# Kernel optimization log

Hardware: AMD Instinct MI355X
Metric: run time of the kernel (lower is better)

The kernel has to match this reference:

```python
import jax, jax.numpy as jnp
import numpy as np

BS = 4096
IN_DIM = 2048
N = 16384          # out_dim / number of labels
K = 32
D = 2 * K + 1      # 65 frequency components (1 DC + K complex pairs)
SLACK = 64
TOTAL_D = D + SLACK
SQRT2 = np.sqrt(2.0).astype(np.float32)


def setup_inputs() -> dict:
    key = jax.random.key(0)
    k1, k2, k3, k4 = jax.random.split(key, 4)
    x = jax.random.normal(k1, (BS, IN_DIM), dtype=jnp.float32)
    # proj: Linear(in_dim, total_D) with bias
    W_proj = jax.random.normal(k2, (TOTAL_D, IN_DIM), dtype=jnp.float32) / np.sqrt(IN_DIM).astype(np.float32)
    b_proj = jnp.zeros((TOTAL_D,), dtype=jnp.float32)
    # use_init: bias[0] = logit(k/N) * sqrt(N)
    mle = K / N
    b0 = np.float32(np.log(mle / (1.0 - mle)) * np.sqrt(N))
    b_proj = b_proj.at[0].set(b0)
    # Ws: Linear(slack_dims, N, bias=False) -> weight (N, slack_dims)
    Ws = jax.random.normal(k3, (N, SLACK), dtype=jnp.float32) / np.sqrt(SLACK).astype(np.float32)
    return {"x": x, "W_proj": W_proj, "b_proj": b_proj, "Ws": Ws}


def reference(x, W_proj, b_proj, Ws):
    bs = x.shape[0]
    h = x @ W_proj.T + b_proj                      # (bs, TOTAL_D)
    # scale cols 1:D by sqrt(2), leave DC and slack cols untouched
    scale = jnp.concatenate([
        jnp.ones((1,), jnp.float32),
        jnp.full((D - 1,), SQRT2, jnp.float32),
        jnp.ones((SLACK,), jnp.float32),
    ])
    h = h * scale
    dc = h[:, 0]                                   # (bs,)
    pairs = h[:, 1:D].reshape(bs, K, 2)            # (bs, K, 2) [real, imag]
    cx = pairs[:, :, 0] - 1j * pairs[:, :, 1]      # conj of complex(real, imag)
    cx = jnp.concatenate([dc[:, None].astype(cx.dtype), cx], axis=1)  # (bs, K+1)
    # zero-padded orthonormal inverse DFT; only real part kept
    yy_dft = jnp.fft.ifft(cx, n=N, norm='ortho', axis=-1).real        # (bs, N)
    yy_slack = h[:, D:] @ Ws.T                     # (bs, N)
    return yy_dft + yy_slack
```

## Files before the change

### kernel.cpp

```cpp
#include <hip/hip_runtime.h>

#define BS 4096
#define IN_DIM 2048
#define NFFT 16384
#define TOTAL_D 129
#define SLACK 64
#define KF 128
#define NPROJ 160
#define SPLITK 8

#define INV_N_SQRT 0.0078125f
#define SC_PAIR 0.011048543456039804f
#define TWO_PI_OVER_N 3.8349519697141029e-4f

typedef __attribute__((ext_vector_type(8))) short bf16x8;
typedef __attribute__((ext_vector_type(4))) float f32x4;

__device__ __forceinline__ ushort f2bf(float f) {
    union { float f; unsigned u; } v; v.f = f;
    unsigned r = v.u + 0x7fffu + ((v.u >> 16) & 1u);
    return (ushort)(r >> 16);
}

__global__ __launch_bounds__(256) void k_basis(const float* __restrict__ Ws,
                                               ushort* __restrict__ Bb) {
    int idx = blockIdx.x * 256 + threadIdx.x;
    int t = idx >> 4, g = idx & 15;
    ushort r[8];
    if (g < 8) {
#pragma unroll
        for (int p = 0; p < 4; ++p) {
            int f = 4 * g + p + 1;
            int phase = (f * t) & (NFFT - 1);
            float ang = (float)phase * TWO_PI_OVER_N;
            float sv, cv;
            __sincosf(ang, &sv, &cv);
            r[2 * p] = f2bf(cv);
            r[2 * p + 1] = f2bf(sv);
        }
    } else {
        const float* w = &Ws[(size_t)t * SLACK + (g - 8) * 8];
        float4 w0 = *(const float4*)w;
        float4 w1 = *(const float4*)(w + 4);
        r[0] = f2bf(w0.x); r[1] = f2bf(w0.y); r[2] = f2bf(w0.z); r[3] = f2bf(w0.w);
        r[4] = f2bf(w1.x); r[5] = f2bf(w1.y); r[6] = f2bf(w1.z); r[7] = f2bf(w1.w);
    }
    ushort4 lo = {r[0], r[1], r[2], r[3]};
    ushort4 hi = {r[4], r[5], r[6], r[7]};
    ushort* dst = &Bb[(size_t)t * KF + g * 8];
    *(ushort4*)dst = lo;
    *(ushort4*)(dst + 4) = hi;
}

__global__ __launch_bounds__(256, 2) void k_proj(const float* __restrict__ x,
                                                 const float* __restrict__ W,
                                                 float* __restrict__ hp) {
    __shared__ ushort As[128 * 40];
    __shared__ ushort Bs[160 * 40];
    const int tid = threadIdx.x;
    const int lane = tid & 63, wave = tid >> 6;
    const int quad = lane >> 4, m = lane & 15;
    const int wm = wave & 1, wn = wave >> 1;
    const int r0 = blockIdx.x * 128;
    const int kbase = blockIdx.y * (IN_DIM / SPLITK);

    f32x4 acc[4][5];
#pragma unroll
    for (int i = 0; i < 4; ++i)
#pragma unroll
        for (int j = 0; j < 5; ++j) acc[i][j] = 0.f;

    for (int ch = 0; ch < IN_DIM / SPLITK / 32; ++ch) {
        const int kb = kbase + ch * 32;
#pragma unroll
        for (int it = 0; it < 4; ++it) {
            int v = tid + it * 256;
            int row = v >> 3, c = v & 7;
            float4 xv = *(const float4*)&x[(size_t)(r0 + row) * IN_DIM + kb + c * 4];
            ushort4 o = {f2bf(xv.x), f2bf(xv.y), f2bf(xv.z), f2bf(xv.w)};
            *(ushort4*)&As[row * 40 + c * 4] = o;
        }
#pragma unroll
        for (int it = 0; it < 5; ++it) {
            int v = tid + it * 256;
            int row = v >> 3, c = v & 7;
            int rw = row < TOTAL_D ? row : TOTAL_D - 1;
            float4 wv = *(const float4*)&W[(size_t)rw * IN_DIM + kb + c * 4];
            ushort4 o = {f2bf(wv.x), f2bf(wv.y), f2bf(wv.z), f2bf(wv.w)};
            *(ushort4*)&Bs[row * 40 + c * 4] = o;
        }
        __syncthreads();
        bf16x8 af[4], bfr[5];
#pragma unroll
        for (int i = 0; i < 4; ++i)
            af[i] = *(const bf16x8*)&As[(wm * 64 + i * 16 + m) * 40 + quad * 8];
#pragma unroll
        for (int j = 0; j < 5; ++j)
            bfr[j] = *(const bf16x8*)&Bs[(wn * 80 + j * 16 + m) * 40 + quad * 8];
#pragma unroll
        for (int i = 0; i < 4; ++i)
#pragma unroll
            for (int j = 0; j < 5; ++j)
                acc[i][j] = __builtin_amdgcn_mfma_f32_16x16x32_bf16(af[i], bfr[j], acc[i][j], 0, 0, 0);
        __syncthreads();
    }
#pragma unroll
    for (int i = 0; i < 4; ++i)
#pragma unroll
        for (int reg = 0; reg < 4; ++reg) {
            int row = r0 + wm * 64 + i * 16 + quad * 4 + reg;
            float* orow = &hp[((size_t)blockIdx.y * BS + row) * NPROJ + wn * 80 + m];
#pragma unroll
            for (int j = 0; j < 5; ++j) orow[j * 16] = acc[i][j][reg];
        }
}

__global__ __launch_bounds__(256) void k_finalize(const float* __restrict__ hp,
                                                  const float* __restrict__ bvec,
                                                  float* __restrict__ dc0,
                                                  ushort* __restrict__ hs) {
    int b = blockIdx.x * 256 + threadIdx.x;
    int g = blockIdx.y;
    int c0 = g * 8;
    float v[8];
#pragma unroll
    for (int e = 0; e < 8; ++e) v[e] = 0.f;
#pragma unroll
    for (int s = 0; s < SPLITK; ++s) {
        const float* p = &hp[((size_t)s * BS + b) * NPROJ + c0];
        float4 p0 = *(const float4*)p;
        float4 p1 = *(const float4*)(p + 4);
        v[0] += p0.x; v[1] += p0.y; v[2] += p0.z; v[3] += p0.w;
        v[4] += p1.x; v[5] += p1.y; v[6] += p1.z; v[7] += p1.w;
    }
#pragma unroll
    for (int e = 0; e < 8; ++e) {
        int c = c0 + e;
        if (c >= TOTAL_D) break;
        float val = v[e] + bvec[c];
        if (c == 0) {
            dc0[b] = val * INV_N_SQRT;
        } else {
            int k = c - 1;
            float sc = (k < 64) ? SC_PAIR : 1.f;
            hs[(size_t)b * KF + k] = f2bf(val * sc);
        }
    }
}

__global__ __launch_bounds__(256, 2) void k_main(const ushort* __restrict__ hs,
                                                 const float* __restrict__ dc0,
                                                 const ushort* __restrict__ Bb,
                                                 float* __restrict__ out) {
    __shared__ ushort As[128 * 128];
    __shared__ ushort Bs[128 * 128];
    const int tid = threadIdx.x;
    const int lane = tid & 63, wave = tid >> 6;
    const int quad = lane >> 4, m = lane & 15;
    const int wm = wave & 1, wn = wave >> 1;
    const int t0 = blockIdx.x * 128;
    const int b0 = blockIdx.y * 128;

#pragma unroll
    for (int it = 0; it < 8; ++it) {
        int v = tid + it * 256;
        int row = v >> 4, g = v & 15;
        uint4 d = *(const uint4*)&Bb[((size_t)(t0 + row) << 7) + g * 8];
        *(uint4*)&As[(row << 7) + ((g ^ (row & 7)) * 8)] = d;
    }
#pragma unroll
    for (int it = 0; it < 8; ++it) {
        int v = tid + it * 256;
        int row = v >> 4, g = v & 15;
        uint4 d = *(const uint4*)&hs[((size_t)(b0 + row) << 7) + g * 8];
        *(uint4*)&Bs[(row << 7) + ((g ^ (row & 7)) * 8)] = d;
    }

    f32x4 acc[4][4];
#pragma unroll
    for (int j = 0; j < 4; ++j) {
        float d = dc0[b0 + wn * 64 + j * 16 + m];
#pragma unroll
        for (int i = 0; i < 4; ++i) acc[i][j] = d;
    }
    __syncthreads();

#pragma unroll
    for (int ks = 0; ks < 4; ++ks) {
        bf16x8 af[4], bfr[4];
#pragma unroll
        for (int i = 0; i < 4; ++i) {
            int row = wm * 64 + i * 16 + m;
            af[i] = *(const bf16x8*)&As[(row << 7) + (((ks * 4 + quad) ^ (row & 7)) * 8)];
        }
#pragma unroll
        for (int j = 0; j < 4; ++j) {
            int row = wn * 64 + j * 16 + m;
            bfr[j] = *(const bf16x8*)&Bs[(row << 7) + (((ks * 4 + quad) ^ (row & 7)) * 8)];
        }
#pragma unroll
        for (int i = 0; i < 4; ++i)
#pragma unroll
            for (int j = 0; j < 4; ++j)
                acc[i][j] = __builtin_amdgcn_mfma_f32_16x16x32_bf16(af[i], bfr[j], acc[i][j], 0, 0, 0);
    }

#pragma unroll
    for (int j = 0; j < 4; ++j) {
        size_t rowb = (size_t)(b0 + wn * 64 + j * 16 + m);
        float* orow = out + rowb * NFFT + t0 + wm * 64 + quad * 4;
#pragma unroll
        for (int i = 0; i < 4; ++i)
            *(f32x4*)&orow[i * 16] = acc[i][j];
    }
}

extern "C" void kernel_launch(void* const* d_in, const int* in_sizes, int n_in,
                              void* d_out, int out_size, void* d_ws, size_t ws_size,
                              hipStream_t stream) {
    const float* x   = (const float*)d_in[0];
    const float* W   = (const float*)d_in[1];
    const float* b   = (const float*)d_in[2];
    const float* Wsl = (const float*)d_in[3];
    float* out = (float*)d_out;

    char* ws = (char*)d_ws;
    float*  h_part = (float*)ws;
    ushort* Bb     = (ushort*)(ws + 20971520);
    ushort* hs     = (ushort*)(ws + 25165824);
    float*  dc0    = (float*)(ws + 26214400);

    k_basis<<<NFFT * 16 / 256, 256, 0, stream>>>(Wsl, Bb);
    k_proj<<<dim3(BS / 128, SPLITK), 256, 0, stream>>>(x, W, h_part);
    k_finalize<<<dim3(BS / 256, 17), 256, 0, stream>>>(h_part, b, dc0, hs);
    k_main<<<dim3(NFFT / 128, BS / 128), 256, 0, stream>>>(hs, dc0, Bb, out);
}
```

Measured before the change: 335.6 us.

## Load GEMM fragments directly from global, remap blocks for XCD locality, nontemporal stores

The output GEMM kernel no longer stages A/B tiles in shared memory. Each wave loads its MFMA fragments straight from global/L2, which removes LDS traffic and the barrier and allows 4 blocks per CU. The grid is flattened and remapped so blocks on the same XCD share basis tiles, and output writes use nontemporal stores to avoid polluting cache. The trade-off is that fragment loads are now redundant across waves and go through global memory with less coalescing.

```diff
diff --git a/kernel.cpp b/kernel.cpp
--- a/kernel.cpp
+++ b/kernel.cpp
@@ -148,33 +148,23 @@
     }
 }
 
-__global__ __launch_bounds__(256, 2) void k_main(const ushort* __restrict__ hs,
+__global__ __launch_bounds__(256, 4) void k_main(const ushort* __restrict__ hs,
                                                  const float* __restrict__ dc0,
                                                  const ushort* __restrict__ Bb,
                                                  float* __restrict__ out) {
-    __shared__ ushort As[128 * 128];
-    __shared__ ushort Bs[128 * 128];
     const int tid = threadIdx.x;
     const int lane = tid & 63, wave = tid >> 6;
     const int quad = lane >> 4, m = lane & 15;
     const int wm = wave & 1, wn = wave >> 1;
-    const int t0 = blockIdx.x * 128;
-    const int b0 = blockIdx.y * 128;
-
-#pragma unroll
-    for (int it = 0; it < 8; ++it) {
-        int v = tid + it * 256;
-        int row = v >> 4, g = v & 15;
-        uint4 d = *(const uint4*)&Bb[((size_t)(t0 + row) << 7) + g * 8];
-        *(uint4*)&As[(row << 7) + ((g ^ (row & 7)) * 8)] = d;
-    }
-#pragma unroll
-    for (int it = 0; it < 8; ++it) {
-        int v = tid + it * 256;
-        int row = v >> 4, g = v & 15;
-        uint4 d = *(const uint4*)&hs[((size_t)(b0 + row) << 7) + g * 8];
-        *(uint4*)&Bs[(row << 7) + ((g ^ (row & 7)) * 8)] = d;
-    }
+
+    int orig = blockIdx.x;
+    int wgid = ((orig & 7) << 9) + (orig >> 3);
+    int tx = wgid >> 5, by = wgid & 31;
+    const int t0 = tx * 128;
+    const int b0 = by * 128;
+
+    const ushort* pA = Bb + (((size_t)(t0 + wm * 64 + m)) << 7) + quad * 8;
+    const ushort* pB = hs + (((size_t)(b0 + wn * 64 + m)) << 7) + quad * 8;
 
     f32x4 acc[4][4];
 #pragma unroll
@@ -183,21 +173,16 @@
 #pragma unroll
         for (int i = 0; i < 4; ++i) acc[i][j] = d;
     }
-    __syncthreads();
 
 #pragma unroll
     for (int ks = 0; ks < 4; ++ks) {
         bf16x8 af[4], bfr[4];
 #pragma unroll
-        for (int i = 0; i < 4; ++i) {
-            int row = wm * 64 + i * 16 + m;
-            af[i] = *(const bf16x8*)&As[(row << 7) + (((ks * 4 + quad) ^ (row & 7)) * 8)];
-        }
-#pragma unroll
-        for (int j = 0; j < 4; ++j) {
-            int row = wn * 64 + j * 16 + m;
-            bfr[j] = *(const bf16x8*)&Bs[(row << 7) + (((ks * 4 + quad) ^ (row & 7)) * 8)];
-        }
+        for (int i = 0; i < 4; ++i)
+            af[i] = *(const bf16x8*)(pA + (size_t)i * 16 * KF + ks * 32);
+#pragma unroll
+        for (int j = 0; j < 4; ++j)
+            bfr[j] = *(const bf16x8*)(pB + (size_t)j * 16 * KF + ks * 32);
 #pragma unroll
         for (int i = 0; i < 4; ++i)
 #pragma unroll
@@ -211,7 +196,7 @@
         float* orow = out + rowb * NFFT + t0 + wm * 64 + quad * 4;
 #pragma unroll
         for (int i = 0; i < 4; ++i)
-            *(f32x4*)&orow[i * 16] = acc[i][j];
+            __builtin_nontemporal_store(acc[i][j], (f32x4*)&orow[i * 16]);
     }
 }
 
@@ -233,5 +218,5 @@
     k_basis<<<NFFT * 16 / 256, 256, 0, stream>>>(Wsl, Bb);
     k_proj<<<dim3(BS / 128, SPLITK), 256, 0, stream>>>(x, W, h_part);
     k_finalize<<<dim3(BS / 256, 17), 256, 0, stream>>>(h_part, b, dc0, hs);
-    k_main<<<dim3(NFFT / 128, BS / 128), 256, 0, stream>>>(hs, dc0, Bb, out);
-}
+    k_main<<<NFFT / 128 * (BS / 128), 256, 0, stream>>>(hs, dc0, Bb, out);
+}
```

Result: slower. 410.3 us (+22.3%).

## Loop k_main over four t-tiles per block with prefetched basis and remapped grid

Applied to the files above, without the earlier changes.

Each k_main block now covers 128 batch rows by 512 output columns. It keeps the hs tile resident in LDS and loops over four basis tiles, loading the next basis tile into registers while the current one is computed and stored. A 1D grid with an XCD-aware block remap groups blocks for L2 locality. This aims to cut redundant hs loads and per-block launch and prologue cost, at the price of extra barriers, higher register pressure and a quarter as many blocks.

```diff
diff --git a/kernel.cpp b/kernel.cpp
--- a/kernel.cpp
+++ b/kernel.cpp
@@ -158,60 +158,93 @@
     const int lane = tid & 63, wave = tid >> 6;
     const int quad = lane >> 4, m = lane & 15;
     const int wm = wave & 1, wn = wave >> 1;
-    const int t0 = blockIdx.x * 128;
-    const int b0 = blockIdx.y * 128;
-
+
+    int orig = blockIdx.x;
+    int wg = ((orig & 7) << 7) + (orig >> 3);
+    const int b0 = (wg & 31) * 128;
+    const int tbase = (wg >> 5) * 512;
+
+    const int srow = tid >> 4;
+    const int sgr = tid & 15;
+
+    uint4 rh[8], rb[8];
 #pragma unroll
     for (int it = 0; it < 8; ++it) {
-        int v = tid + it * 256;
-        int row = v >> 4, g = v & 15;
-        uint4 d = *(const uint4*)&Bb[((size_t)(t0 + row) << 7) + g * 8];
-        *(uint4*)&As[(row << 7) + ((g ^ (row & 7)) * 8)] = d;
+        int row = srow + it * 16;
+        rh[it] = *(const uint4*)&hs[((size_t)(b0 + row) << 7) + sgr * 8];
     }
 #pragma unroll
     for (int it = 0; it < 8; ++it) {
-        int v = tid + it * 256;
-        int row = v >> 4, g = v & 15;
-        uint4 d = *(const uint4*)&hs[((size_t)(b0 + row) << 7) + g * 8];
-        *(uint4*)&Bs[(row << 7) + ((g ^ (row & 7)) * 8)] = d;
-    }
-
-    f32x4 acc[4][4];
-#pragma unroll
-    for (int j = 0; j < 4; ++j) {
-        float d = dc0[b0 + wn * 64 + j * 16 + m];
-#pragma unroll
-        for (int i = 0; i < 4; ++i) acc[i][j] = d;
-    }
+        int row = srow + it * 16;
+        rb[it] = *(const uint4*)&Bb[((size_t)(tbase + row) << 7) + sgr * 8];
+    }
+#pragma unroll
+    for (int it = 0; it < 8; ++it) {
+        int row = srow + it * 16;
+        int gx = (sgr ^ (row & 7)) * 8;
+        *(uint4*)&Bs[(row << 7) + gx] = rh[it];
+        *(uint4*)&As[(row << 7) + gx] = rb[it];
+    }
+    float dc[4];
+#pragma unroll
+    for (int j = 0; j < 4; ++j) dc[j] = dc0[b0 + wn * 64 + j * 16 + m];
     __syncthreads();
 
-#pragma unroll
-    for (int ks = 0; ks < 4; ++ks) {
-        bf16x8 af[4], bfr[4];
-#pragma unroll
-        for (int i = 0; i < 4; ++i) {
-            int row = wm * 64 + i * 16 + m;
-            af[i] = *(const bf16x8*)&As[(row << 7) + (((ks * 4 + quad) ^ (row & 7)) * 8)];
-        }
+#pragma unroll 1
+    for (int i = 0; i < 4; ++i) {
+        const int t0 = tbase + i * 128;
+        if (i < 3) {
+#pragma unroll
+            for (int it = 0; it < 8; ++it) {
+                int row = srow + it * 16;
+                rb[it] = *(const uint4*)&Bb[((size_t)(t0 + 128 + row) << 7) + sgr * 8];
+            }
+        }
+
+        f32x4 acc[4][4];
+#pragma unroll
+        for (int j = 0; j < 4; ++j)
+#pragma unroll
+            for (int ii = 0; ii < 4; ++ii) acc[ii][j] = dc[j];
+
+#pragma unroll
+        for (int ks = 0; ks < 4; ++ks) {
+            bf16x8 af[4], bfr[4];
+#pragma unroll
+            for (int ii = 0; ii < 4; ++ii) {
+                int row = wm * 64 + ii * 16 + m;
+                af[ii] = *(const bf16x8*)&As[(row << 7) + (((ks * 4 + quad) ^ (row & 7)) * 8)];
+            }
+#pragma unroll
+            for (int j = 0; j < 4; ++j) {
+                int row = wn * 64 + j * 16 + m;
+                bfr[j] = *(const bf16x8*)&Bs[(row << 7) + (((ks * 4 + quad) ^ (row & 7)) * 8)];
+            }
+#pragma unroll
+            for (int ii = 0; ii < 4; ++ii)
+#pragma unroll
+                for (int j = 0; j < 4; ++j)
+                    acc[ii][j] = __builtin_amdgcn_mfma_f32_16x16x32_bf16(af[ii], bfr[j], acc[ii][j], 0, 0, 0);
+        }
+
 #pragma unroll
         for (int j = 0; j < 4; ++j) {
-            int row = wn * 64 + j * 16 + m;
-            bfr[j] = *(const bf16x8*)&Bs[(row << 7) + (((ks * 4 + quad) ^ (row & 7)) * 8)];
-        }
-#pragma unroll
-        for (int i = 0; i < 4; ++i)
-#pragma unroll
-            for (int j = 0; j < 4; ++j)
-                acc[i][j] = __builtin_amdgcn_mfma_f32_16x16x32_bf16(af[i], bfr[j], acc[i][j], 0, 0, 0);
-    }
-
-#pragma unroll
-    for (int j = 0; j < 4; ++j) {
-        size_t rowb = (size_t)(b0 + wn * 64 + j * 16 + m);
-        float* orow = out + rowb * NFFT + t0 + wm * 64 + quad * 4;
-#pragma unroll
-        for (int i = 0; i < 4; ++i)
-            *(f32x4*)&orow[i * 16] = acc[i][j];
+            size_t rowb = (size_t)(b0 + wn * 64 + j * 16 + m);
+            float* orow = out + rowb * NFFT + t0 + wm * 64 + quad * 4;
+#pragma unroll
+            for (int ii = 0; ii < 4; ++ii)
+                *(f32x4*)&orow[ii * 16] = acc[ii][j];
+        }
+
+        if (i < 3) {
+            __syncthreads();
+#pragma unroll
+            for (int it = 0; it < 8; ++it) {
+                int row = srow + it * 16;
+                *(uint4*)&As[(row << 7) + ((sgr ^ (row & 7)) * 8)] = rb[it];
+            }
+            __syncthreads();
+        }
     }
 }
 
@@ -233,5 +266,5 @@
     k_basis<<<NFFT * 16 / 256, 256, 0, stream>>>(Wsl, Bb);
     k_proj<<<dim3(BS / 128, SPLITK), 256, 0, stream>>>(x, W, h_part);
     k_finalize<<<dim3(BS / 256, 17), 256, 0, stream>>>(h_part, b, dc0, hs);
-    k_main<<<dim3(NFFT / 128, BS / 128), 256, 0, stream>>>(hs, dc0, Bb, out);
-}
+    k_main<<<BS / 128 * (NFFT / 512), 256, 0, stream>>>(hs, dc0, Bb, out);
+}
```

Measured after the change: 396.1 us. +18.0%, slower.

## Fuse projection and finalize into one kernel, dropping split-K partial buffer

Applied to the files above, without the earlier changes.

Replaces the split-K projection GEMM and separate reduction/finalize kernel with one kernel in which each block computes 32 rows over the full K dimension and applies bias, scaling and bf16 conversion in its epilogue. This removes the 21MB partial-sum write and re-read and one launch. The trade-off is that every block now re-reads and re-converts the full W_proj matrix (160x2048) from global memory, with only 128 blocks and no split-K parallelism, so the W traffic grows and the per-block serial K loop is longer.

```diff
diff --git a/kernel.cpp b/kernel.cpp
--- a/kernel.cpp
+++ b/kernel.cpp
@@ -6,8 +6,6 @@
 #define TOTAL_D 129
 #define SLACK 64
 #define KF 128
-#define NPROJ 160
-#define SPLITK 8
 
 #define INV_N_SQRT 0.0078125f
 #define SC_PAIR 0.011048543456039804f
@@ -52,98 +50,71 @@
     *(ushort4*)(dst + 4) = hi;
 }
 
-__global__ __launch_bounds__(256, 2) void k_proj(const float* __restrict__ x,
+__global__ __launch_bounds__(256) void k_projfin(const float* __restrict__ x,
                                                  const float* __restrict__ W,
-                                                 float* __restrict__ hp) {
-    __shared__ ushort As[128 * 40];
-    __shared__ ushort Bs[160 * 40];
+                                                 const float* __restrict__ bvec,
+                                                 float* __restrict__ dc0,
+                                                 ushort* __restrict__ hs) {
+    __shared__ ushort As[32 * 72];
+    __shared__ ushort Bs[160 * 72];
     const int tid = threadIdx.x;
     const int lane = tid & 63, wave = tid >> 6;
     const int quad = lane >> 4, m = lane & 15;
     const int wm = wave & 1, wn = wave >> 1;
-    const int r0 = blockIdx.x * 128;
-    const int kbase = blockIdx.y * (IN_DIM / SPLITK);
-
-    f32x4 acc[4][5];
-#pragma unroll
-    for (int i = 0; i < 4; ++i)
-#pragma unroll
-        for (int j = 0; j < 5; ++j) acc[i][j] = 0.f;
-
-    for (int ch = 0; ch < IN_DIM / SPLITK / 32; ++ch) {
-        const int kb = kbase + ch * 32;
-#pragma unroll
-        for (int it = 0; it < 4; ++it) {
+    const int r0 = blockIdx.x * 32;
+
+    f32x4 acc[5];
+#pragma unroll
+    for (int j = 0; j < 5; ++j) acc[j] = 0.f;
+
+    for (int kb = 0; kb < IN_DIM; kb += 64) {
+#pragma unroll
+        for (int it = 0; it < 2; ++it) {
             int v = tid + it * 256;
-            int row = v >> 3, c = v & 7;
+            int row = v >> 4, c = v & 15;
             float4 xv = *(const float4*)&x[(size_t)(r0 + row) * IN_DIM + kb + c * 4];
             ushort4 o = {f2bf(xv.x), f2bf(xv.y), f2bf(xv.z), f2bf(xv.w)};
-            *(ushort4*)&As[row * 40 + c * 4] = o;
-        }
-#pragma unroll
-        for (int it = 0; it < 5; ++it) {
+            *(ushort4*)&As[row * 72 + c * 4] = o;
+        }
+#pragma unroll
+        for (int it = 0; it < 10; ++it) {
             int v = tid + it * 256;
-            int row = v >> 3, c = v & 7;
+            int row = v >> 4, c = v & 15;
             int rw = row < TOTAL_D ? row : TOTAL_D - 1;
             float4 wv = *(const float4*)&W[(size_t)rw * IN_DIM + kb + c * 4];
             ushort4 o = {f2bf(wv.x), f2bf(wv.y), f2bf(wv.z), f2bf(wv.w)};
-            *(ushort4*)&Bs[row * 40 + c * 4] = o;
+            *(ushort4*)&Bs[row * 72 + c * 4] = o;
         }
         __syncthreads();
-        bf16x8 af[4], bfr[5];
-#pragma unroll
-        for (int i = 0; i < 4; ++i)
-            af[i] = *(const bf16x8*)&As[(wm * 64 + i * 16 + m) * 40 + quad * 8];
-#pragma unroll
-        for (int j = 0; j < 5; ++j)
-            bfr[j] = *(const bf16x8*)&Bs[(wn * 80 + j * 16 + m) * 40 + quad * 8];
-#pragma unroll
-        for (int i = 0; i < 4; ++i)
+#pragma unroll
+        for (int ks = 0; ks < 2; ++ks) {
+            bf16x8 af = *(const bf16x8*)&As[(wm * 16 + m) * 72 + ks * 32 + quad * 8];
+            bf16x8 bfr[5];
 #pragma unroll
             for (int j = 0; j < 5; ++j)
-                acc[i][j] = __builtin_amdgcn_mfma_f32_16x16x32_bf16(af[i], bfr[j], acc[i][j], 0, 0, 0);
+                bfr[j] = *(const bf16x8*)&Bs[(wn * 80 + j * 16 + m) * 72 + ks * 32 + quad * 8];
+#pragma unroll
+            for (int j = 0; j < 5; ++j)
+                acc[j] = __builtin_amdgcn_mfma_f32_16x16x32_bf16(af, bfr[j], acc[j], 0, 0, 0);
+        }
         __syncthreads();
     }
 #pragma unroll
-    for (int i = 0; i < 4; ++i)
+    for (int j = 0; j < 5; ++j) {
+        int c = wn * 80 + j * 16 + m;
+        if (c >= TOTAL_D) continue;
+        float bias = bvec[c];
 #pragma unroll
         for (int reg = 0; reg < 4; ++reg) {
-            int row = r0 + wm * 64 + i * 16 + quad * 4 + reg;
-            float* orow = &hp[((size_t)blockIdx.y * BS + row) * NPROJ + wn * 80 + m];
-#pragma unroll
-            for (int j = 0; j < 5; ++j) orow[j * 16] = acc[i][j][reg];
-        }
-}
-
-__global__ __launch_bounds__(256) void k_finalize(const float* __restrict__ hp,
-                                                  const float* __restrict__ bvec,
-                                                  float* __restrict__ dc0,
-                                                  ushort* __restrict__ hs) {
-    int b = blockIdx.x * 256 + threadIdx.x;
-    int g = blockIdx.y;
-    int c0 = g * 8;
-    float v[8];
-#pragma unroll
-    for (int e = 0; e < 8; ++e) v[e] = 0.f;
-#pragma unroll
-    for (int s = 0; s < SPLITK; ++s) {
-        const float* p = &hp[((size_t)s * BS + b) * NPROJ + c0];
-        float4 p0 = *(const float4*)p;
-        float4 p1 = *(const float4*)(p + 4);
-        v[0] += p0.x; v[1] += p0.y; v[2] += p0.z; v[3] += p0.w;
-        v[4] += p1.x; v[5] += p1.y; v[6] += p1.z; v[7] += p1.w;
-    }
-#pragma unroll
-    for (int e = 0; e < 8; ++e) {
-        int c = c0 + e;
-        if (c >= TOTAL_D) break;
-        float val = v[e] + bvec[c];
-        if (c == 0) {
-            dc0[b] = val * INV_N_SQRT;
-        } else {
-            int k = c - 1;
-            float sc = (k < 64) ? SC_PAIR : 1.f;
-            hs[(size_t)b * KF + k] = f2bf(val * sc);
+            int row = r0 + wm * 16 + quad * 4 + reg;
+            float val = acc[j][reg] + bias;
+            if (c == 0) {
+                dc0[row] = val * INV_N_SQRT;
+            } else {
+                int k = c - 1;
+                float sc = (k < 64) ? SC_PAIR : 1.f;
+                hs[(size_t)row * KF + k] = f2bf(val * sc);
+            }
         }
     }
 }
@@ -225,13 +196,11 @@
     float* out = (float*)d_out;
 
     char* ws = (char*)d_ws;
-    float*  h_part = (float*)ws;
-    ushort* Bb     = (ushort*)(ws + 20971520);
-    ushort* hs     = (ushort*)(ws + 25165824);
-    float*  dc0    = (float*)(ws + 26214400);
+    ushort* Bb  = (ushort*)ws;
+    ushort* hs  = (ushort*)(ws + 4194304);
+    float*  dc0 = (float*)(ws + 5242880);
 
     k_basis<<<NFFT * 16 / 256, 256, 0, stream>>>(Wsl, Bb);
-    k_proj<<<dim3(BS / 128, SPLITK), 256, 0, stream>>>(x, W, h_part);
-    k_finalize<<<dim3(BS / 256, 17), 256, 0, stream>>>(h_part, b, dc0, hs);
+    k_projfin<<<BS / 32, 256, 0, stream>>>(x, W, b, dc0, hs);
     k_main<<<dim3(NFFT / 128, BS / 128), 256, 0, stream>>>(hs, dc0, Bb, out);
 }
```

Result: slower. 466.4 us (+39.0%).
